# Optimization experiments

Measured on AMD Instinct MI355X. Metric: run time of the kernel, lower is better.

## Reference

```python
import jax, jax.numpy as jnp
import numpy as np

B, S, D, DOM, L = 16, 512, 512, 8, 3  # batch, seq_len, mem_dim (S==D required by outputs*rel), domains, layers


def setup_inputs() -> dict:
    key = jax.random.key(0)
    ks = jax.random.split(key, 16)
    adj = jax.random.uniform(ks[0], (B, S, S), jnp.float32)
    rel = jax.random.uniform(ks[1], (B, S, S), jnp.float32)
    gcn_inputs = jax.random.normal(ks[2], (B, S, D), jnp.float32)
    frontrel = jax.random.normal(ks[3], (B, S, D), jnp.float32)
    backrel = jax.random.normal(ks[4], (B, S, D), jnp.float32)
    # depmap: exactly one selected column per (b, row) so masked_select reshapes to [B,S]
    depmap = jax.nn.one_hot(jax.random.randint(ks[5], (B, S), 0, S), S, dtype=jnp.float32)
    dom_idx = jax.random.randint(ks[6], (B, S), 0, DOM)
    has_dom = jax.random.bernoulli(ks[7], 0.5, (B, S)).astype(jnp.float32)
    domain_id = jax.nn.one_hot(dom_idx, DOM, dtype=jnp.float32) * has_dom[..., None]
    redom_idx = jax.random.randint(ks[8], (B, S), 0, DOM)
    has_re = jax.random.bernoulli(ks[9], 0.5, (B, S)).astype(jnp.float32)
    redomain_id = jax.nn.one_hot(redom_idx, DOM, dtype=jnp.float32) * has_re[..., None]
    domain = jax.random.bernoulli(ks[10], 0.5, (B, S, DOM, 1))
    mask = jnp.ones((B, S), dtype=bool)
    sc = 1.0 / np.sqrt(D)
    W_layers = jax.random.normal(ks[11], (L, D, D), jnp.float32) * sc
    b_layers = jnp.zeros((L, D), jnp.float32)
    prelu_a = jnp.full((L,), 0.25, jnp.float32)  # nn.PReLU default
    W_dg = jax.random.normal(ks[12], (D, D), jnp.float32) * sc
    b_dg = jnp.zeros((D,), jnp.float32)
    W_mg = jax.random.normal(ks[13], (2 * D, D), jnp.float32) * (1.0 / np.sqrt(2 * D))
    b_mg = jnp.zeros((D,), jnp.float32)
    W_out = jax.random.normal(ks[14], (L * D, D), jnp.float32) * (1.0 / np.sqrt(L * D))
    b_out = jnp.zeros((D,), jnp.float32)
    return dict(adj=adj, domain=domain, domain_id=domain_id, redomain_id=redomain_id,
                frontrel=frontrel, backrel=backrel, depmap=depmap, rel=rel,
                gcn_inputs=gcn_inputs, mask=mask, W_layers=W_layers, b_layers=b_layers,
                prelu_a=prelu_a, W_dg=W_dg, b_dg=b_dg, W_mg=W_mg, b_mg=b_mg,
                W_out=W_out, b_out=b_out)


def _forward(adj, domain, domain_id, redomain_id, frontrel, backrel, depmap, rel,
             gcn_inputs, W_layers, b_layers, prelu_a, W_dg, b_dg, W_mg, b_mg, W_out, b_out):
    denom = jnp.sum(adj, axis=2, keepdims=True) + 1.0                     # [B,S,1]
    domain_mask = jnp.sum(domain_id, axis=-1, keepdims=True) == 1.0       # [B,S,1]
    redomain_mask = jnp.sum(redomain_id, axis=-1, keepdims=True) == 1.0   # [B,S,1]
    frontadj = jnp.sum(adj * depmap, axis=-1)                             # [B,S]
    backadj = jnp.sum(jnp.swapaxes(adj, -1, -2) * depmap, axis=-1)        # [B,S]
    outputs = gcn_inputs
    outs = []
    for l in range(L):
        frontoutputs = jnp.where(domain_mask, 0.0, outputs)
        backoutputs = jnp.where(redomain_mask, 0.0, jnp.einsum('bij,bjd->bid', rel, outputs))
        # domain pooling: mask then max over sequence -> [B,DOM,D]
        pooled = jnp.max(jnp.where(domain, -10000.0, outputs[:, :, None, :]), axis=1)
        domain_outputs = jax.nn.sigmoid(pooled @ W_dg + b_dg)             # domain_gate
        frontoutputs = frontoutputs + jnp.einsum('bsk,bkd->bsd', domain_id, domain_outputs)
        backoutputs = backoutputs + jnp.einsum('bsk,bkd->bsd', redomain_id, domain_outputs)
        frontdepadj = jax.nn.sigmoid(jnp.concatenate([frontoutputs, frontrel], -1) @ W_mg + b_mg)
        backdepadj = jax.nn.sigmoid(jnp.concatenate([backoutputs, backrel], -1) @ W_mg + b_mg)
        delta = jnp.einsum('bji,bjd->bid', rel, frontadj[..., None] * frontdepadj * frontoutputs)
        delta = delta + backadj[..., None] * backdepadj * backoutputs
        Ax = jnp.einsum('bij,bjd->bid', adj, outputs * rel)               # requires S==D
        AxW = (Ax @ W_layers[l] + b_layers[l]) + (outputs @ W_layers[l] + b_layers[l]) + delta
        x = AxW / denom
        outputs = jnp.where(x >= 0, x, prelu_a[l] * x)                    # PReLU
        outs.append(outputs)                                              # dropout is eval-mode identity
    gcn_outputs = jnp.concatenate(outs, axis=2)                           # [B,S,L*D]
    return gcn_outputs @ W_out + b_out + gcn_inputs


def reference(adj, domain, domain_id, redomain_id, frontrel, backrel, depmap, rel,
              gcn_inputs, mask, W_layers, b_layers, prelu_a, W_dg, b_dg, W_mg, b_mg,
              W_out, b_out):
    return _forward(adj, domain, domain_id, redomain_id, frontrel, backrel, depmap, rel,
                    gcn_inputs, W_layers, b_layers, prelu_a, W_dg, b_dg, W_mg, b_mg,
                    W_out, b_out)
```

## Files before the change

### kernel.cpp

```cpp
#include <hip/hip_runtime.h>
#include <math.h>

#define SD_  (512*512)
#define BSD_ (16*512*512)

typedef unsigned short u16;
typedef short s16x8 __attribute__((ext_vector_type(8)));
typedef float f32x4 __attribute__((ext_vector_type(4)));

__device__ __forceinline__ float sigmoidf_(float x) { return 1.0f / (1.0f + __expf(-x)); }

__device__ __forceinline__ u16 f2bf(float f) {
    unsigned int u = __float_as_uint(f);
    u += 0x7fffu + ((u >> 16) & 1u);
    return (u16)(u >> 16);
}
__device__ __forceinline__ float bf2f(u16 h) { return __uint_as_float((unsigned)h << 16); }

__device__ __forceinline__ void glds16(const void* g, void* l) {
    __builtin_amdgcn_global_load_lds((const __attribute__((address_space(1))) unsigned int*)g,
                                     (__attribute__((address_space(3))) unsigned int*)l, 16, 0, 0);
}

struct GP {
    const u16 *A1, *A2;  int lda1, lda2;  long sA;
    const u16 *B1, *B2;  int ldb1, ldb2;  long sB;
    void *C1, *C2;  int obf1, obf2, ldc1, ldc2;  long sC;
    u16 *CT1, *CT2;  long sCT;
    const void *Ci1, *Ci2;  int cm1, cm2, ldci1, ldci2;  long sCi1, sCi2;
    const float *bias;  float bS;
    const float *sc1, *sc2;
    const int *selm1, *seli1, *selm2, *seli2;
    const u16 *DG;
    const float *invden, *prelu;  int pidx;
    int M, K, zs, swzX, swzY;
};

template<int EPI, int ASEL>
__global__ __launch_bounds__(512, 4)
void gemm3(const GP p)
{
    __shared__ short LS[32768];
    const int tid = threadIdx.x;
    int bx, by, bz;
    if (p.swzX >= 0) {
        const int bid = blockIdx.x + gridDim.x * (blockIdx.y + gridDim.y * blockIdx.z);
        const int ppx = (gridDim.y * gridDim.z) >> 3;
        const int xcd = bid & 7, idx = bid >> 3;
        const int pair = xcd * ppx + (idx >> p.swzX);
        bx = idx & ((1 << p.swzX) - 1);
        by = pair & ((1 << p.swzY) - 1);
        bz = pair >> p.swzY;
    } else { bx = blockIdx.x; by = blockIdx.y; bz = blockIdx.z; }

    const int seg = (bz >= p.zs) ? 1 : 0;
    const int z = seg ? bz - p.zs : bz;
    const u16* Ab = (seg ? p.A2 : p.A1) + z * p.sA;
    const int lda = seg ? p.lda2 : p.lda1;
    const u16* Bb = (seg ? p.B2 : p.B1) + z * p.sB;
    const int ldb = seg ? p.ldb2 : p.ldb1;

    const int m0 = by * 128, n0 = bx * 128;
    const int srow = ((tid >> 6) << 4) | (tid & 15);
    const int sk0 = ((tid >> 4) & 3) << 3;
    const int slot = ((srow >> 4) << 9) + (sk0 << 4) + ((srow & 15) << 3);

    const u16* aRow = Ab + (long)(m0 + srow) * lda + sk0;
    if (ASEL) {
        const int* selm = seg ? p.selm2 : p.selm1;
        const int* seli = seg ? p.seli2 : p.seli1;
        const int r0 = m0 + srow;
        if (selm[r0]) aRow = p.DG + (long)(((r0 >> 9) << 3) + seli[r0]) * 512 + sk0;
    }
    const u16* bRow = Bb + (long)(n0 + srow) * ldb + sk0;

    auto stage = [&](int kb2) {
        short* base = &LS[(kb2 & 1) * 16384];
        const int kk = kb2 << 6;
        glds16(aRow + kk,      &base[slot]);
        glds16(aRow + kk + 32, &base[4096 + slot]);
        glds16(bRow + kk,      &base[8192 + slot]);
        glds16(bRow + kk + 32, &base[12288 + slot]);
    };

    const int wave = tid >> 6, lane = tid & 63;
    const int gA = (wave >> 2) << 2;
    const int gB = (wave & 3) << 1;

    f32x4 acc[4][2] = {};
    const int nkb = p.K >> 6;

    stage(0);
    for (int kb = 0; kb < nkb; ++kb) {
        if (kb + 1 < nkb) {
            stage(kb + 1);
            asm volatile("s_waitcnt vmcnt(4)" ::: "memory");
        } else {
            asm volatile("s_waitcnt vmcnt(0)" ::: "memory");
        }
        __builtin_amdgcn_s_barrier();
        const short* ls = &LS[(kb & 1) * 16384];
#pragma unroll
        for (int kh = 0; kh < 2; ++kh) {
            s16x8 aF[4], bF[2];
#pragma unroll
            for (int mt = 0; mt < 4; ++mt) aF[mt] = *(const s16x8*)&ls[kh * 4096 + ((gA + mt) * 64 + lane) * 8];
#pragma unroll
            for (int nt = 0; nt < 2; ++nt) bF[nt] = *(const s16x8*)&ls[8192 + kh * 4096 + ((gB + nt) * 64 + lane) * 8];
#pragma unroll
            for (int mt = 0; mt < 4; ++mt)
#pragma unroll
                for (int nt = 0; nt < 2; ++nt)
                    acc[mt][nt] = __builtin_amdgcn_mfma_f32_16x16x32_bf16(aF[mt], bF[nt], acc[mt][nt], 0, 0, 0);
        }
        __builtin_amdgcn_s_barrier();
    }

    const int ml = lane & 15, quad = lane >> 4;
    const int wm = (wave >> 2) * 64, wn = (wave & 3) * 32;
    u16* Cb16 = (u16*)(seg ? p.C2 : p.C1);
    float* Cb32 = (float*)(seg ? p.C2 : p.C1);
    const int haveC = (seg ? p.C2 : p.C1) != nullptr;
    const int obf = seg ? p.obf2 : p.obf1;
    const int ldc = seg ? p.ldc2 : p.ldc1;
    if (haveC) { if (obf) Cb16 += z * p.sC; else Cb32 += z * p.sC; }
    u16* CTb = seg ? p.CT2 : p.CT1;
    if (CTb) CTb += z * p.sCT;
    const u16* CiT = (const u16*)(seg ? p.Ci2 : p.Ci1);
    const float* Ci32 = (const float*)(seg ? p.Ci2 : p.Ci1);
    const int cm = seg ? p.cm2 : p.cm1;
    const int ldci = seg ? p.ldci2 : p.ldci1;
    {
        const long sCi = seg ? p.sCi2 : p.sCi1;
        if (cm) CiT += z * sCi; else Ci32 += z * sCi;
    }
    const float pal = (EPI == 4) ? p.prelu[p.pidx] : 0.0f;
    const float* scp = (EPI == 8) ? (seg ? p.sc2 : p.sc1) : nullptr;
    const int* eselm = (EPI == 8) ? (seg ? p.selm2 : p.selm1) : nullptr;
    const int* eseli2 = (EPI == 8) ? (seg ? p.seli2 : p.seli1) : nullptr;

    const bool useEp = haveC && (obf == 1);
    u16* epbuf = (u16*)LS;
    if (useEp) __syncthreads();

#pragma unroll
    for (int mt = 0; mt < 4; ++mt) {
#pragma unroll
        for (int nt = 0; nt < 2; ++nt) {
            const int col = n0 + wn + nt * 16 + ml;
            const int rowb = m0 + wm + mt * 16 + quad * 4;
            float cin4[4];
            if (EPI == 3 || EPI == 4 || EPI == 7 || EPI == 8) {
                if (cm) {
                    const ushort4 c4 = *(const ushort4*)&CiT[(long)(rowb >> 9) * SD_ + (long)col * 512 + (rowb & 511)];
                    cin4[0] = bf2f(c4.x); cin4[1] = bf2f(c4.y); cin4[2] = bf2f(c4.z); cin4[3] = bf2f(c4.w);
                } else {
#pragma unroll
                    for (int r = 0; r < 4; ++r) cin4[r] = Ci32[(long)(rowb + r) * ldci + col];
                }
            }
            u16 pk[4];
#pragma unroll
            for (int r = 0; r < 4; ++r) {
                const int row = rowb + r;
                float x = acc[mt][nt][r];
                if (EPI == 1) x += p.bias[col];
                else if (EPI == 3) x += cin4[r];
                else if (EPI == 4) {
                    x = (x + p.bS * p.bias[col] + cin4[r]) * p.invden[z * p.M + row];
                    x = (x >= 0.0f) ? x : pal * x;
                }
                else if (EPI == 6) x = sigmoidf_(x + p.bias[col]);
                else if (EPI == 7) x += p.bias[col] + cin4[r];
                else if (EPI == 8) {
                    float av;
                    if (eselm[row]) av = bf2f(p.DG[(long)(((row >> 9) << 3) + eseli2[row]) * 512 + col]);
                    else av = bf2f(Ab[(long)row * lda + col]);
                    x = sigmoidf_(x + cin4[r]) * scp[row] * av;
                }
                if (haveC && obf == 0) Cb32[(long)row * ldc + col] = x;
                pk[r] = f2bf(x);
                if (useEp) epbuf[(wm + mt * 16 + quad * 4 + r) * 136 + wn + nt * 16 + ml] = pk[r];
            }
            if (CTb) {
                u16* ct = CTb + (long)(rowb >> 9) * SD_ + (long)col * 512 + (rowb & 511);
                *(ushort4*)ct = *(ushort4*)pk;
            }
        }
    }
    if (useEp) {
        __syncthreads();
        const int lr = tid >> 2, cs = (tid & 3) * 32;
#pragma unroll
        for (int j = 0; j < 4; ++j) {
            const s16x8 v = *(const s16x8*)&epbuf[lr * 136 + cs + j * 8];
            *(s16x8*)&Cb16[(long)(m0 + lr) * ldc + n0 + cs + j * 8] = v;
        }
    }
}

__global__ __launch_bounds__(256)
void cvt_k(const float* __restrict__ s, u16* __restrict__ d)
{
    const long i = ((long)blockIdx.x * 256 + threadIdx.x) * 4;
    const float4 v = *(const float4*)&s[i];
    ushort4 h = { f2bf(v.x), f2bf(v.y), f2bf(v.z), f2bf(v.w) };
    *(ushort4*)&d[i] = h;
}

__global__ __launch_bounds__(256)
void trcvt_k(const float* __restrict__ src, u16* __restrict__ dstT, u16* __restrict__ dstN,
             const int R, const int C, const long sS, const long sDT, const long sDN)
{
    __shared__ u16 t[64][72];
    const float* s = src + blockIdx.z * sS;
    const int r0 = blockIdx.y * 64, c0 = blockIdx.x * 64;
    const int tid = threadIdx.x;
    const int lr = tid >> 2, lc4 = (tid & 3) * 16;
#pragma unroll
    for (int j = 0; j < 4; ++j) {
        const float4 v = *(const float4*)&s[(long)(r0 + lr) * C + c0 + lc4 + j * 4];
        ushort4 h = { f2bf(v.x), f2bf(v.y), f2bf(v.z), f2bf(v.w) };
        *(ushort4*)&t[lr][lc4 + j * 4] = h;
        if (dstN) *(ushort4*)&dstN[blockIdx.z * sDN + (long)(r0 + lr) * C + c0 + lc4 + j * 4] = h;
    }
    __syncthreads();
    const int lcol = tid >> 2, rc = (tid & 3) * 16;
#pragma unroll
    for (int j = 0; j < 2; ++j) {
        s16x8 v;
#pragma unroll
        for (int q = 0; q < 8; ++q) v[q] = (short)t[rc + j * 8 + q][lcol];
        *(s16x8*)&dstT[blockIdx.z * sDT + (long)(c0 + lcol) * R + r0 + rc + j * 8] = v;
    }
}

__global__ __launch_bounds__(256)
void e0_k(const float* __restrict__ adj, const float* __restrict__ depmap,
          const float* __restrict__ domain_id, const float* __restrict__ redomain_id,
          float* __restrict__ invden, float* __restrict__ fa, int* __restrict__ dcol,
          int* __restrict__ dm, int* __restrict__ dsel, int* __restrict__ rm, int* __restrict__ rsel)
{
    const int bs = blockIdx.x;
    const int t = threadIdx.x;
    const float* arow = adj + (long)bs * 512;
    const float* drow = depmap + (long)bs * 512;
    __shared__ float red[256];
    __shared__ int scol;
    if (t == 0) scol = 0;
    const float a0 = arow[t], a1 = arow[t + 256];
    const float p0 = drow[t], p1 = drow[t + 256];
    if (p0 > 0.5f) scol = t;
    if (p1 > 0.5f) scol = t + 256;
    red[t] = a0 + a1;
    __syncthreads();
    for (int off = 128; off > 0; off >>= 1) { if (t < off) red[t] += red[t + off]; __syncthreads(); }
    if (t == 0) invden[bs] = 1.0f / (red[0] + 1.0f);
    __syncthreads();
    red[t] = a0 * p0 + a1 * p1;
    __syncthreads();
    for (int off = 128; off > 0; off >>= 1) { if (t < off) red[t] += red[t + off]; __syncthreads(); }
    if (t == 0) {
        fa[bs] = red[0];
        dcol[bs] = scol;
        const float* q = domain_id + (long)bs * 8;
        float s = 0.f; int sel = 0;
        for (int k = 0; k < 8; ++k) { float v = q[k]; s += v; if (v > 0.5f) sel = k; }
        dm[bs] = (s > 0.5f) ? 1 : 0; dsel[bs] = sel;
        const float* r = redomain_id + (long)bs * 8;
        s = 0.f; sel = 0;
        for (int k = 0; k < 8; ++k) { float v = r[k]; s += v; if (v > 0.5f) sel = k; }
        rm[bs] = (s > 0.5f) ? 1 : 0; rsel[bs] = sel;
    }
}

__global__ void e0b_k(const float* __restrict__ adj, const int* __restrict__ dcol, float* __restrict__ ba)
{
    const int bs = blockIdx.x * 256 + threadIdx.x;
    const int b = bs >> 9, s = bs & 511;
    ba[bs] = adj[((long)b * 512 + dcol[bs]) * 512 + s];
}

__global__ __launch_bounds__(256)
void pool1_k(const u16* __restrict__ OUT, const int ldO, const int* __restrict__ domain,
             const u16* __restrict__ relb, u16* __restrict__ cm, u16* __restrict__ OxRT)
{
    const int b = blockIdx.x >> 4, c = blockIdx.x & 15;
    const int s0 = c * 32, tid = threadIdx.x;
    __shared__ int dom[256];
    dom[tid] = domain[((long)(b * 512 + s0 + (tid >> 3))) * 8 + (tid & 7)];
    __syncthreads();
    const int d0 = tid * 2;
    float mxa[8], mxb[8];
#pragma unroll
    for (int k = 0; k < 8; ++k) { mxa[k] = -10000.0f; mxb[k] = -10000.0f; }
    s16x8 pA[4], pB[4];
#pragma unroll
    for (int s = 0; s < 32; ++s) {
        const int row = b * 512 + s0 + s;
        const unsigned uv = *(const unsigned*)&OUT[(long)row * ldO + d0];
        const unsigned rv = *(const unsigned*)&relb[(long)row * 512 + d0];
        const float vx = bf2f((u16)(uv & 0xffff)), vy = bf2f((u16)(uv >> 16));
        const float rx = bf2f((u16)(rv & 0xffff)), ry = bf2f((u16)(rv >> 16));
        pA[s >> 3][s & 7] = (short)f2bf(vx * rx);
        pB[s >> 3][s & 7] = (short)f2bf(vy * ry);
        const int* ds = &dom[s * 8];
#pragma unroll
        for (int k = 0; k < 8; ++k) {
            mxa[k] = fmaxf(mxa[k], ds[k] ? -10000.0f : vx);
            mxb[k] = fmaxf(mxb[k], ds[k] ? -10000.0f : vy);
        }
    }
#pragma unroll
    for (int j = 0; j < 4; ++j) *(s16x8*)&OxRT[((long)b * 512 + d0) * 512 + s0 + j * 8] = pA[j];
#pragma unroll
    for (int j = 0; j < 4; ++j) *(s16x8*)&OxRT[((long)b * 512 + d0 + 1) * 512 + s0 + j * 8] = pB[j];
#pragma unroll
    for (int k = 0; k < 8; ++k) {
        ushort2 h = { f2bf(mxa[k]), f2bf(mxb[k]) };
        *(ushort2*)&cm[((long)((b * 16 + c) * 8 + k)) * 512 + d0] = h;
    }
}

__global__ void pool2_k(const u16* __restrict__ cm, u16* __restrict__ pooled)
{
    const int q = blockIdx.x * 256 + threadIdx.x;
    const int b = q >> 12, k = (q >> 9) & 7, d = q & 511;
    float m = -1e30f;
    for (int c = 0; c < 16; ++c)
        m = fmaxf(m, bf2f(cm[((long)((b * 16 + c) * 8 + k)) * 512 + d]));
    pooled[((long)(b * 8 + k)) * 512 + d] = f2bf(m);
}

extern "C" void kernel_launch(void* const* d_in, const int* in_sizes, int n_in,
                              void* d_out, int out_size, void* d_ws, size_t ws_size,
                              hipStream_t stream)
{
    const float* adj         = (const float*)d_in[0];
    const int*   domain      = (const int*)d_in[1];
    const float* domain_id   = (const float*)d_in[2];
    const float* redomain_id = (const float*)d_in[3];
    const float* frontrel    = (const float*)d_in[4];
    const float* backrel     = (const float*)d_in[5];
    const float* depmap      = (const float*)d_in[6];
    const float* rel         = (const float*)d_in[7];
    const float* gcn         = (const float*)d_in[8];
    const float* W_layers    = (const float*)d_in[10];
    const float* b_layers    = (const float*)d_in[11];
    const float* prelu_a     = (const float*)d_in[12];
    const float* W_dg        = (const float*)d_in[13];
    const float* b_dg        = (const float*)d_in[14];
    const float* W_mg        = (const float*)d_in[15];
    const float* b_mg        = (const float*)d_in[16];
    const float* W_out       = (const float*)d_in[17];
    const float* b_out       = (const float*)d_in[18];
    float* out = (float*)d_out;

    char* w = (char*)d_ws;
    auto alloc = [&](size_t bytes) { void* p = (void*)w; w += (bytes + 255) & ~(size_t)255; return p; };
    const size_t Bb = (size_t)BSD_ * 2;
    u16* OUTS_bf = (u16*)alloc((size_t)8192 * 1536 * 2);
    u16* OUTT    = (u16*)alloc(Bb);
    u16* gcnT    = (u16*)alloc(Bb);
    u16* RB_bf   = (u16*)alloc(Bb);
    u16* XBT     = (u16*)alloc(Bb);
    u16* XFT     = (u16*)alloc(Bb);
    u16* OxRT    = (u16*)alloc(Bb);
    u16* DLT     = (u16*)alloc(Bb);
    u16* AXO_bf  = (u16*)alloc(Bb);
    u16* BBT     = (u16*)alloc(Bb);
    u16* FBT     = (u16*)alloc(Bb);
    u16* rel_bf  = (u16*)alloc(Bb);
    u16* relT_bf = (u16*)alloc(Bb);
    u16* adj_bf  = (u16*)alloc(Bb);
    u16* gcn_bf  = (u16*)alloc(Bb);
    u16* frel_bf = (u16*)alloc(Bb);
    u16* brel_bf = (u16*)alloc(Bb);
    u16* WmgT1 = (u16*)alloc((size_t)SD_ * 2);
    u16* WmgT2 = (u16*)alloc((size_t)SD_ * 2);
    u16* WdgT  = (u16*)alloc((size_t)SD_ * 2);
    u16* WlT   = (u16*)alloc((size_t)3 * SD_ * 2);
    u16* WoutT = (u16*)alloc((size_t)512 * 1536 * 2);
    u16* cm     = (u16*)alloc((size_t)16 * 16 * 8 * 512 * 2);
    u16* pooled = (u16*)alloc((size_t)16 * 8 * 512 * 2);
    u16* DGb    = (u16*)alloc((size_t)16 * 8 * 512 * 2);
    float* invden = (float*)alloc(8192 * 4);
    float* fa     = (float*)alloc(8192 * 4);
    float* ba     = (float*)alloc(8192 * 4);
    int* dcol = (int*)alloc(8192 * 4);
    int* dm   = (int*)alloc(8192 * 4);
    int* dsel = (int*)alloc(8192 * 4);
    int* rm   = (int*)alloc(8192 * 4);
    int* rsel = (int*)alloc(8192 * 4);

    cvt_k<<<4096, 256, 0, stream>>>(adj, adj_bf);
    cvt_k<<<4096, 256, 0, stream>>>(frontrel, frel_bf);
    cvt_k<<<4096, 256, 0, stream>>>(backrel, brel_bf);
    trcvt_k<<<dim3(8, 8, 16), 256, 0, stream>>>(gcn, gcnT, gcn_bf, 512, 512, SD_, SD_, SD_);
    trcvt_k<<<dim3(8, 8, 16), 256, 0, stream>>>(rel, relT_bf, rel_bf, 512, 512, SD_, SD_, SD_);
    trcvt_k<<<dim3(8, 8, 1), 256, 0, stream>>>(W_mg, WmgT1, nullptr, 512, 512, 0, 0, 0);
    trcvt_k<<<dim3(8, 8, 1), 256, 0, stream>>>(W_mg + SD_, WmgT2, nullptr, 512, 512, 0, 0, 0);
    trcvt_k<<<dim3(8, 8, 1), 256, 0, stream>>>(W_dg, WdgT, nullptr, 512, 512, 0, 0, 0);
    trcvt_k<<<dim3(8, 8, 3), 256, 0, stream>>>(W_layers, WlT, nullptr, 512, 512, SD_, SD_, 0);
    trcvt_k<<<dim3(8, 24, 1), 256, 0, stream>>>(W_out, WoutT, nullptr, 1536, 512, 0, 0, 0);
    e0_k<<<8192, 256, 0, stream>>>(adj, depmap, domain_id, redomain_id, invden, fa, dcol, dm, dsel, rm, rsel);
    e0b_k<<<32, 256, 0, stream>>>(adj, dcol, ba);

    const dim3 blk(512);

    {
        GP p{};
        p.A1 = brel_bf; p.A2 = frel_bf; p.lda1 = p.lda2 = 512; p.sA = 0;
        p.B1 = p.B2 = WmgT2; p.ldb1 = p.ldb2 = 512; p.sB = 0;
        p.CT1 = BBT; p.CT2 = FBT; p.sCT = 0;
        p.bias = b_mg; p.M = 8192; p.K = 512; p.zs = 1; p.swzX = 2; p.swzY = 6;
        gemm3<1, 0><<<dim3(4, 64, 2), blk, 0, stream>>>(p);
    }

    for (int l = 0; l < 3; ++l) {
        const u16* OUTp  = (l == 0) ? gcn_bf : (OUTS_bf + (l - 1) * 512);
        const u16* OUTTp = (l == 0) ? gcnT : OUTT;
        const int ldO = (l == 0) ? 512 : 1536;

        {
            GP p{};
            p.A1 = rel_bf; p.lda1 = 512; p.sA = SD_;
            p.B1 = OUTTp; p.ldb1 = 512; p.sB = SD_;
            p.C1 = RB_bf; p.obf1 = 1; p.ldc1 = 512; p.sC = SD_;
            p.M = 512; p.K = 512; p.zs = 16; p.swzX = 2; p.swzY = 2;
            gemm3<0, 0><<<dim3(4, 4, 16), blk, 0, stream>>>(p);
        }
        pool1_k<<<256, 256, 0, stream>>>(OUTp, ldO, domain, rel_bf, cm, OxRT);
        pool2_k<<<256, 256, 0, stream>>>(cm, pooled);
        {
            GP p{};
            p.A1 = pooled; p.lda1 = 512; p.B1 = WdgT; p.ldb1 = 512;
            p.C1 = DGb; p.obf1 = 1; p.ldc1 = 512;
            p.bias = b_dg; p.M = 128; p.K = 512; p.zs = 1; p.swzX = -1;
            gemm3<6, 0><<<dim3(4, 1, 1), blk, 0, stream>>>(p);
        }
        {
            GP p{};
            p.A1 = RB_bf; p.lda1 = 512; p.A2 = OUTp; p.lda2 = ldO; p.sA = 0;
            p.selm1 = rm; p.seli1 = rsel; p.selm2 = dm; p.seli2 = dsel; p.DG = DGb;
            p.B1 = p.B2 = WmgT1; p.ldb1 = p.ldb2 = 512; p.sB = 0;
            p.Ci1 = BBT; p.Ci2 = FBT; p.cm1 = p.cm2 = 1; p.ldci1 = p.ldci2 = 512; p.sCi1 = p.sCi2 = 0;
            p.CT1 = XBT; p.CT2 = XFT; p.sCT = 0;
            p.sc1 = ba; p.sc2 = fa; p.M = 8192; p.K = 512; p.zs = 1; p.swzX = 2; p.swzY = 6;
            gemm3<8, 1><<<dim3(4, 64, 2), blk, 0, stream>>>(p);
        }
        {
            GP p{};
            p.A1 = relT_bf; p.lda1 = 512; p.A2 = adj_bf; p.lda2 = 512; p.sA = SD_;
            p.B1 = XFT; p.ldb1 = 512;
            p.B2 = OxRT; p.ldb2 = 512; p.sB = SD_;
            p.Ci1 = XBT; p.cm1 = 1; p.ldci1 = 512; p.sCi1 = SD_;
            p.Ci2 = OUTTp; p.cm2 = 1; p.ldci2 = 512; p.sCi2 = SD_;
            p.CT1 = DLT; p.sCT = SD_;
            p.C2 = AXO_bf; p.obf2 = 1; p.ldc2 = 512; p.sC = SD_;
            p.M = 512; p.K = 512; p.zs = 16; p.swzX = 2; p.swzY = 2;
            gemm3<3, 0><<<dim3(4, 4, 32), blk, 0, stream>>>(p);
        }
        {
            GP p{};
            p.A1 = AXO_bf; p.lda1 = 512; p.sA = SD_;
            p.B1 = WlT + (long)l * SD_; p.ldb1 = 512; p.sB = 0;
            p.Ci1 = DLT; p.cm1 = 1; p.ldci1 = 512; p.sCi1 = SD_;
            p.C1 = OUTS_bf + l * 512; p.obf1 = 1; p.ldc1 = 1536; p.sC = (long)512 * 1536;
            p.CT1 = OUTT; p.sCT = SD_;
            p.bias = b_layers + l * 512; p.bS = 2.0f;
            p.invden = invden; p.prelu = prelu_a; p.pidx = l;
            p.M = 512; p.K = 512; p.zs = 16; p.swzX = 2; p.swzY = 2;
            gemm3<4, 0><<<dim3(4, 4, 16), blk, 0, stream>>>(p);
        }
    }

    {
        GP p{};
        p.A1 = OUTS_bf; p.lda1 = 1536; p.sA = 0;
        p.B1 = WoutT; p.ldb1 = 1536; p.sB = 0;
        p.Ci1 = gcn; p.cm1 = 0; p.ldci1 = 512; p.sCi1 = 0;
        p.C1 = out; p.obf1 = 0; p.ldc1 = 512; p.sC = 0;
        p.bias = b_out; p.M = 8192; p.K = 1536; p.zs = 1; p.swzX = 2; p.swzY = 6;
        gemm3<7, 0><<<dim3(4, 64, 1), blk, 0, stream>>>(p);
    }
}
```

Measured before the change: 682.8 us.

## Interleave per-chunk async LDS loads with MFMA phases and raise MFMA priority

Splits each K-block of the bf16 GEMM main loop into four phases. Each phase issues one of the next block's global-to-LDS loads, waits only on the matching earlier load, then runs a small group of MFMAs. This spreads memory issue across the compute and raises wave priority around the MFMA groups with s_setprio. The aim is finer-grained overlap of loads and matrix ops. The cost is four barriers per K-block instead of two, plus more fragile vmcnt bookkeeping.

```diff
diff --git a/kernel.cpp b/kernel.cpp
--- a/kernel.cpp
+++ b/kernel.cpp
@@ -74,15 +74,6 @@
     }
     const u16* bRow = Bb + (long)(n0 + srow) * ldb + sk0;
 
-    auto stage = [&](int kb2) {
-        short* base = &LS[(kb2 & 1) * 16384];
-        const int kk = kb2 << 6;
-        glds16(aRow + kk,      &base[slot]);
-        glds16(aRow + kk + 32, &base[4096 + slot]);
-        glds16(bRow + kk,      &base[8192 + slot]);
-        glds16(bRow + kk + 32, &base[12288 + slot]);
-    };
-
     const int wave = tid >> 6, lane = tid & 63;
     const int gA = (wave >> 2) << 2;
     const int gB = (wave & 3) << 1;
@@ -90,30 +81,86 @@
     f32x4 acc[4][2] = {};
     const int nkb = p.K >> 6;
 
-    stage(0);
+    {
+        short* b0 = &LS[0];
+        glds16(aRow + 0,  &b0[slot]);
+        glds16(bRow + 0,  &b0[8192 + slot]);
+        glds16(aRow + 32, &b0[4096 + slot]);
+        glds16(bRow + 32, &b0[12288 + slot]);
+    }
+
     for (int kb = 0; kb < nkb; ++kb) {
-        if (kb + 1 < nkb) {
-            stage(kb + 1);
-            asm volatile("s_waitcnt vmcnt(4)" ::: "memory");
+        const short* ls = &LS[(kb & 1) * 16384];
+        short* nb = &LS[((kb + 1) & 1) * 16384];
+        const int kk = (kb + 1) << 6;
+        const bool more = (kb + 1 < nkb);
+        s16x8 aF[4], bF[2];
+
+        if (more) {
+            glds16(aRow + kk, &nb[slot]);
+            asm volatile("s_waitcnt vmcnt(3)" ::: "memory");
+        } else {
+            asm volatile("s_waitcnt vmcnt(2)" ::: "memory");
+        }
+        __builtin_amdgcn_s_barrier();
+        aF[0] = *(const s16x8*)&ls[((gA + 0) * 64 + lane) * 8];
+        aF[1] = *(const s16x8*)&ls[((gA + 1) * 64 + lane) * 8];
+        bF[0] = *(const s16x8*)&ls[8192 + ((gB + 0) * 64 + lane) * 8];
+        bF[1] = *(const s16x8*)&ls[8192 + ((gB + 1) * 64 + lane) * 8];
+        __builtin_amdgcn_s_setprio(1);
+        acc[0][0] = __builtin_amdgcn_mfma_f32_16x16x32_bf16(aF[0], bF[0], acc[0][0], 0, 0, 0);
+        acc[0][1] = __builtin_amdgcn_mfma_f32_16x16x32_bf16(aF[0], bF[1], acc[0][1], 0, 0, 0);
+        acc[1][0] = __builtin_amdgcn_mfma_f32_16x16x32_bf16(aF[1], bF[0], acc[1][0], 0, 0, 0);
+        acc[1][1] = __builtin_amdgcn_mfma_f32_16x16x32_bf16(aF[1], bF[1], acc[1][1], 0, 0, 0);
+        __builtin_amdgcn_s_setprio(0);
+
+        if (more) {
+            glds16(bRow + kk, &nb[8192 + slot]);
+            asm volatile("s_waitcnt vmcnt(3)" ::: "memory");
+        } else {
+            asm volatile("s_waitcnt vmcnt(2)" ::: "memory");
+        }
+        __builtin_amdgcn_s_barrier();
+        aF[2] = *(const s16x8*)&ls[((gA + 2) * 64 + lane) * 8];
+        aF[3] = *(const s16x8*)&ls[((gA + 3) * 64 + lane) * 8];
+        __builtin_amdgcn_s_setprio(1);
+        acc[2][0] = __builtin_amdgcn_mfma_f32_16x16x32_bf16(aF[2], bF[0], acc[2][0], 0, 0, 0);
+        acc[2][1] = __builtin_amdgcn_mfma_f32_16x16x32_bf16(aF[2], bF[1], acc[2][1], 0, 0, 0);
+        acc[3][0] = __builtin_amdgcn_mfma_f32_16x16x32_bf16(aF[3], bF[0], acc[3][0], 0, 0, 0);
+        acc[3][1] = __builtin_amdgcn_mfma_f32_16x16x32_bf16(aF[3], bF[1], acc[3][1], 0, 0, 0);
+        __builtin_amdgcn_s_setprio(0);
+
+        if (more) {
+            glds16(aRow + kk + 32, &nb[4096 + slot]);
+            asm volatile("s_waitcnt vmcnt(3)" ::: "memory");
         } else {
             asm volatile("s_waitcnt vmcnt(0)" ::: "memory");
         }
         __builtin_amdgcn_s_barrier();
-        const short* ls = &LS[(kb & 1) * 16384];
-#pragma unroll
-        for (int kh = 0; kh < 2; ++kh) {
-            s16x8 aF[4], bF[2];
-#pragma unroll
-            for (int mt = 0; mt < 4; ++mt) aF[mt] = *(const s16x8*)&ls[kh * 4096 + ((gA + mt) * 64 + lane) * 8];
-#pragma unroll
-            for (int nt = 0; nt < 2; ++nt) bF[nt] = *(const s16x8*)&ls[8192 + kh * 4096 + ((gB + nt) * 64 + lane) * 8];
-#pragma unroll
-            for (int mt = 0; mt < 4; ++mt)
-#pragma unroll
-                for (int nt = 0; nt < 2; ++nt)
-                    acc[mt][nt] = __builtin_amdgcn_mfma_f32_16x16x32_bf16(aF[mt], bF[nt], acc[mt][nt], 0, 0, 0);
+        aF[0] = *(const s16x8*)&ls[4096 + ((gA + 0) * 64 + lane) * 8];
+        aF[1] = *(const s16x8*)&ls[4096 + ((gA + 1) * 64 + lane) * 8];
+        bF[0] = *(const s16x8*)&ls[12288 + ((gB + 0) * 64 + lane) * 8];
+        bF[1] = *(const s16x8*)&ls[12288 + ((gB + 1) * 64 + lane) * 8];
+        __builtin_amdgcn_s_setprio(1);
+        acc[0][0] = __builtin_amdgcn_mfma_f32_16x16x32_bf16(aF[0], bF[0], acc[0][0], 0, 0, 0);
+        acc[0][1] = __builtin_amdgcn_mfma_f32_16x16x32_bf16(aF[0], bF[1], acc[0][1], 0, 0, 0);
+        acc[1][0] = __builtin_amdgcn_mfma_f32_16x16x32_bf16(aF[1], bF[0], acc[1][0], 0, 0, 0);
+        acc[1][1] = __builtin_amdgcn_mfma_f32_16x16x32_bf16(aF[1], bF[1], acc[1][1], 0, 0, 0);
+        __builtin_amdgcn_s_setprio(0);
+
+        if (more) {
+            glds16(bRow + kk + 32, &nb[12288 + slot]);
+            asm volatile("s_waitcnt vmcnt(3)" ::: "memory");
         }
         __builtin_amdgcn_s_barrier();
+        aF[2] = *(const s16x8*)&ls[4096 + ((gA + 2) * 64 + lane) * 8];
+        aF[3] = *(const s16x8*)&ls[4096 + ((gA + 3) * 64 + lane) * 8];
+        __builtin_amdgcn_s_setprio(1);
+        acc[2][0] = __builtin_amdgcn_mfma_f32_16x16x32_bf16(aF[2], bF[0], acc[2][0], 0, 0, 0);
+        acc[2][1] = __builtin_amdgcn_mfma_f32_16x16x32_bf16(aF[2], bF[1], acc[2][1], 0, 0, 0);
+        acc[3][0] = __builtin_amdgcn_mfma_f32_16x16x32_bf16(aF[3], bF[0], acc[3][0], 0, 0, 0);
+        acc[3][1] = __builtin_amdgcn_mfma_f32_16x16x32_bf16(aF[3], bF[1], acc[3][1], 0, 0, 0);
+        __builtin_amdgcn_s_setprio(0);
     }
 
     const int ml = lane & 15, quad = lane >> 4;
```

Measured after the change: 681.1 us. About the same (-0.2%).
